# Performance work log

Measured on AMD Instinct MI355X. Metric: run time of the kernel, lower is better.

The kernel has to match this reference:

```python
import jax, jax.numpy as jnp
import numpy as np

K = 20          # neighbour_num
EMB = 512       # emb_dims
EPS = 1e-12     # guards sqrt grad at self-neighbor zero distance


def setup_inputs() -> dict:
    key = jax.random.key(0)
    ks = jax.random.split(key, 6)
    B, D, N = 8, 3, 4096
    C_in = 2 * D + K  # 26 = 6 + neighbour_num
    def xavier(k, o, c):
        return jax.random.normal(k, (o, c), jnp.float32) * jnp.sqrt(2.0 / (o + c))
    return {
        "x":  jax.random.normal(ks[0], (B, D, N), jnp.float32),
        "w1": xavier(ks[1], 64, C_in),
        "w2": xavier(ks[2], 64, 64),
        "w3": xavier(ks[3], 128, 64),
        "w4": xavier(ks[4], 256, 128),
        "w5": xavier(ks[5], EMB, 512),
    }


def _graph_feature(x):
    # x: (B, D, N). Returns (B, 2D+K, N, K).
    B, D, N = x.shape
    xt = jnp.swapaxes(x, 1, 2)                      # (B, N, D)
    sq = jnp.sum(x * x, axis=1)                     # (B, N)
    # pairwise = -||xi - xj||^2 ; topk picks nearest neighbors (incl. self)
    pair = 2.0 * jnp.einsum('bdn,bdm->bnm', x, x) - sq[:, :, None] - sq[:, None, :]
    idx = jax.lax.top_k(pair, K)[1]                 # (B, N, K) int32
    nbr = xt[jnp.arange(B)[:, None, None], idx]     # (B, N, K, D) gather
    xc = jnp.broadcast_to(xt[:, :, None, :], (B, N, K, D))
    dist = jnp.sqrt(jnp.sum((nbr - xc) ** 2, axis=-1) + EPS)   # (B, N, K)
    distr = jnp.broadcast_to(dist[:, :, None, :], (B, N, K, K))
    feat = jnp.concatenate([xc, nbr, distr], axis=-1)          # (B, N, K, 2D+K)
    return jnp.transpose(feat, (0, 3, 1, 2))        # (B, 2D+K, N, K)


def _conv1x1(h, w):
    # h: (B, C, N, K), w: (O, C)  -> (B, O, N, K)
    return jnp.einsum('bcnk,oc->bonk', h, w)


def reference(x, w1, w2, w3, w4, w5):
    h = _graph_feature(x)                           # (B, 26, N, K)
    h = jax.nn.relu(_conv1x1(h, w1)); x1 = h.max(axis=-1)   # (B, 64, N)
    h = jax.nn.relu(_conv1x1(h, w2)); x2 = h.max(axis=-1)   # (B, 64, N)
    h = jax.nn.relu(_conv1x1(h, w3)); x3 = h.max(axis=-1)   # (B, 128, N)
    h = jax.nn.relu(_conv1x1(h, w4)); x4 = h.max(axis=-1)   # (B, 256, N)
    cat = jnp.concatenate([x1, x2, x3, x4], axis=1)          # (B, 512, N)
    out = jax.nn.relu(jnp.einsum('bcn,oc->bon', cat, w5))    # (B, EMB, N)
    return out
```

## Files before the change

### kernel.cpp

```cpp
#include <hip/hip_runtime.h>
#include <cstdint>
#include <cstddef>

#define NB   8
#define NPTS 4096
#define KNN  20
#define P    4
#define QPW  4

typedef __attribute__((ext_vector_type(8))) short    short8;
typedef __attribute__((ext_vector_type(4))) float    floatx4;
typedef __attribute__((ext_vector_type(4))) unsigned short ushort4v;

__device__ __forceinline__ uint16_t f2bf(float f) {
    uint32_t u = __float_as_uint(f);
    uint32_t r = (u + 0x7FFFu + ((u >> 16) & 1u)) >> 16;
    return (uint16_t)r;
}
__device__ __forceinline__ float bf2f(uint16_t h) {
    return __uint_as_float(((uint32_t)h) << 16);
}

#define NEGINF __int_as_float((int)0xFF800000)

template <int CTRL>
__device__ __forceinline__ float dpp_maxf(float v) {
    int o = __builtin_amdgcn_update_dpp(__float_as_int(v), __float_as_int(v),
                                        CTRL, 0xF, 0xF, false);
    return fmaxf(v, __int_as_float(o));
}
__device__ __forceinline__ float wave_max_f32(float v) {
    v = dpp_maxf<0x111>(v);
    v = dpp_maxf<0x112>(v);
    v = dpp_maxf<0x114>(v);
    v = dpp_maxf<0x118>(v);
    v = dpp_maxf<0x142>(v);
    v = dpp_maxf<0x143>(v);
    return __int_as_float(__builtin_amdgcn_readlane(__float_as_int(v), 63));
}

__global__ __launch_bounds__(256) void prep_xyzs(
    const float* __restrict__ x,
    float4* __restrict__ xyzs)
{
    const int i = blockIdx.x * 256 + threadIdx.x;
    if (i >= NB * NPTS) return;
    const int b = i / NPTS, n = i - b * NPTS;
    const float* xb = x + (size_t)b * 3 * NPTS;
    const float x0 = xb[n], x1 = xb[NPTS + n], x2 = xb[2 * NPTS + n];
    float4 v;
    v.x = x0; v.y = x1; v.z = x2;
    v.w = fmaf(x2, x2, fmaf(x1, x1, x0 * x0));
    xyzs[i] = v;
}

__global__ __launch_bounds__(256) void topk_kernel(
    const float4* __restrict__ xyzs,
    int*   __restrict__ idx_out,
    float* __restrict__ dist_out)
{
    const int t = threadIdx.x;
    const int wave = t >> 6, l = t & 63;
    const int nbase = (blockIdx.x * 4 + wave) * QPW;
    const int b = blockIdx.y;
    const float4* xq = xyzs + (size_t)b * NPTS;

    float xn0[QPW], xn1[QPW], xn2[QPW], sqn[QPW];
    float V0[QPW], V1[QPW], V2[QPW];
    int   J0[QPW], J1[QPW], J2[QPW];
    unsigned long long consumed[QPW];
    int   my_m[QPW];

    #pragma unroll
    for (int p = 0; p < QPW; ++p) {
        const float4 pn = xq[nbase + p];
        xn0[p] = pn.x; xn1[p] = pn.y; xn2[p] = pn.z; sqn[p] = pn.w;
        V0[p] = NEGINF; V1[p] = NEGINF; V2[p] = NEGINF;
        J0[p] = 0; J1[p] = 0; J2[p] = 0;
        consumed[p] = 0ull;
        my_m[p] = 0;
    }

    #pragma unroll 4
    for (int j = 0; j < 64; ++j) {
        const float4 pm = xq[j * 64 + l];
        #pragma unroll
        for (int p = 0; p < QPW; ++p) {
            const float dot = fmaf(xn2[p], pm.z, fmaf(xn1[p], pm.y, xn0[p] * pm.x));
            const float s = 2.0f * dot - sqn[p] - pm.w;
            const bool c0 = s > V0[p], c1 = s > V1[p], c2 = s > V2[p];
            const float nV2 = __builtin_amdgcn_fmed3f(V1[p], V2[p], s);
            const float nV1 = __builtin_amdgcn_fmed3f(V0[p], V1[p], s);
            V0[p] = fmaxf(V0[p], s);
            V1[p] = nV1; V2[p] = nV2;
            const int tA = c1 ? J1[p] : j;
            J2[p] = c2 ? tA : J2[p];
            const int tB = c0 ? J0[p] : j;
            J1[p] = c1 ? tB : J1[p];
            J0[p] = c0 ? j : J0[p];
        }
    }

    #pragma unroll
    for (int p = 0; p < QPW; ++p) {
        for (int k = 0; k < KNN; ++k) {
            if (V0[p] == NEGINF) {
                V1[p] = NEGINF; V2[p] = NEGINF;
                for (int j = 0; j < 64; ++j) {
                    const float4 pm = xq[j * 64 + l];
                    const float dot = fmaf(xn2[p], pm.z, fmaf(xn1[p], pm.y, xn0[p] * pm.x));
                    float s = 2.0f * dot - sqn[p] - pm.w;
                    if ((consumed[p] >> j) & 1ull) s = NEGINF;
                    const bool c0 = s > V0[p], c1 = s > V1[p], c2 = s > V2[p];
                    const float nV2 = __builtin_amdgcn_fmed3f(V1[p], V2[p], s);
                    const float nV1 = __builtin_amdgcn_fmed3f(V0[p], V1[p], s);
                    V0[p] = fmaxf(V0[p], s);
                    V1[p] = nV1; V2[p] = nV2;
                    const int tA = c1 ? J1[p] : j;
                    J2[p] = c2 ? tA : J2[p];
                    const int tB = c0 ? J0[p] : j;
                    J1[p] = c1 ? tB : J1[p];
                    J0[p] = c0 ? j : J0[p];
                }
            }
            const float w = wave_max_f32(V0[p]);
            const unsigned long long own = __ballot(V0[p] == w);
            const int owner = (int)__builtin_ctzll(own);
            const int jwin  = __builtin_amdgcn_readlane(J0[p], owner);
            const int m     = jwin * 64 + owner;
            if (l == k) my_m[p] = m;
            if (l == owner) {
                consumed[p] |= 1ull << J0[p];
                V0[p] = V1[p]; V1[p] = V2[p]; V2[p] = NEGINF;
                J0[p] = J1[p]; J1[p] = J2[p];
            }
        }
    }

    #pragma unroll
    for (int p = 0; p < QPW; ++p) {
        if (l < KNN) {
            const int n = nbase + p;
            const float4 pm = xq[my_m[p]];
            const float d0 = pm.x - xn0[p], d1 = pm.y - xn1[p], d2 = pm.z - xn2[p];
            const float dist = sqrtf(((d0 * d0 + d1 * d1) + d2 * d2) + 1e-12f);
            const size_t base = ((size_t)b * NPTS + n) * KNN + l;
            idx_out[base]  = my_m[p];
            dist_out[base] = dist;
        }
    }
}

__global__ void prep_wfrag(const float* __restrict__ w, uint16_t* __restrict__ frag,
                           int C, int NT, int KT) {
    const int i = blockIdx.x * 256 + threadIdx.x;
    if (i >= NT * KT * 64) return;
    const int lane = i & 63;
    const int kt   = (i >> 6) % KT;
    const int nt   = (i >> 6) / KT;
    const int n    = nt * 16 + (lane & 15);
    const int c0   = kt * 32 + (lane >> 4) * 8;
    uint16_t o[8];
    #pragma unroll
    for (int j = 0; j < 8; ++j) {
        const int c = c0 + j;
        o[j] = (c < C) ? f2bf(w[(size_t)n * C + c]) : (uint16_t)0;
    }
    uint16_t* dst = frag + (size_t)i * 8;
    #pragma unroll
    for (int j = 0; j < 8; ++j) dst[j] = o[j];
}

__global__ __launch_bounds__(256) void prep_w5bf(const float* __restrict__ w5,
                                                 uint16_t* __restrict__ w5b) {
    const int i = blockIdx.x * 256 + threadIdx.x;
    if (i < 512 * 512) w5b[i] = f2bf(w5[i]);
}

template <int NT_TOT, int KT, int IN_STRIDE, int OUT_STRIDE>
__device__ __forceinline__ void mfma_layer(const uint16_t* __restrict__ in,
                                           uint16_t* __restrict__ out,
                                           const uint16_t* __restrict__ wf,
                                           int wave, int lane) {
    constexpr int NT_W = NT_TOT / 4;
    const int col = lane & 15, quad = lane >> 4;
    short8 bfrag[NT_W][KT];
    #pragma unroll
    for (int ni = 0; ni < NT_W; ++ni)
        #pragma unroll
        for (int k = 0; k < KT; ++k)
            bfrag[ni][k] = *(const short8*)(wf +
                ((size_t)((wave * NT_W + ni) * KT + k) * 64 + lane) * 8);
    #pragma unroll
    for (int mt = 0; mt < 5; ++mt) {
        short8 af[KT];
        #pragma unroll
        for (int k = 0; k < KT; ++k)
            af[k] = *(const short8*)(in + (mt * 16 + col) * IN_STRIDE + k * 32 + quad * 8);
        #pragma unroll
        for (int ni = 0; ni < NT_W; ++ni) {
            floatx4 acc = {0.f, 0.f, 0.f, 0.f};
            #pragma unroll
            for (int k = 0; k < KT; ++k)
                acc = __builtin_amdgcn_mfma_f32_16x16x32_bf16(af[k], bfrag[ni][k], acc, 0, 0, 0);
            const int nt = wave * NT_W + ni;
            #pragma unroll
            for (int r = 0; r < 4; ++r) {
                const float v = acc[r] > 0.f ? acc[r] : 0.f;
                out[(mt * 16 + quad * 4 + r) * OUT_STRIDE + nt * 16 + col] = f2bf(v);
            }
        }
    }
}

template <int O, int STRIDE>
__device__ __forceinline__ void maxk(const uint16_t* __restrict__ h,
                                     uint16_t* __restrict__ cat_ws, int catoff,
                                     int t, int b, int n0) {
    constexpr int G = O / 8;
    if (t < P * G) {
        const int p = t / G, g = t % G;
        uint16_t mx[8];
        #pragma unroll
        for (int j = 0; j < 8; ++j) mx[j] = 0;
        for (int k = 0; k < KNN; ++k) {
            const uint16_t* row = h + (p * KNN + k) * STRIDE + g * 8;
            #pragma unroll
            for (int j = 0; j < 8; ++j) mx[j] = row[j] > mx[j] ? row[j] : mx[j];
        }
        uint16_t* dst = cat_ws + ((size_t)b * NPTS + n0 + p) * 512 + catoff + g * 8;
        *(short8*)dst = *(const short8*)mx;
    }
}

__global__ __launch_bounds__(256) void fused_mlp_mfma(
    const float* __restrict__ x,
    const int*   __restrict__ idx_ws,
    const float* __restrict__ dist_ws,
    const uint16_t* __restrict__ wf1,
    const uint16_t* __restrict__ wf2,
    const uint16_t* __restrict__ wf3,
    const uint16_t* __restrict__ wf4,
    uint16_t* __restrict__ cat_ws)
{
    const int n0 = blockIdx.x * P, b = blockIdx.y, t = threadIdx.x;
    const int wave = t >> 6, lane = t & 63;

    __shared__ __align__(16) uint16_t bufA[12800];
    __shared__ __align__(16) uint16_t bufB[10880];

    for (int i = t; i < 1600; i += 256) ((uint32_t*)bufA)[i] = 0;
    __syncthreads();
    {
        const float* xb = x + (size_t)b * 3 * NPTS;
        if (t < P * KNN) {
            const int p = t / KNN, k = t % KNN;
            const int n = n0 + p;
            const size_t base = ((size_t)b * NPTS + n) * KNN + k;
            const int   m = idx_ws[base];
            const float d = dist_ws[base];
            uint16_t* fr = bufA + t * 40;
            fr[0] = f2bf(xb[n]);        fr[1] = f2bf(xb[NPTS + n]);
            fr[2] = f2bf(xb[2 * NPTS + n]);
            fr[3] = f2bf(xb[m]);        fr[4] = f2bf(xb[NPTS + m]);
            fr[5] = f2bf(xb[2 * NPTS + m]);
            const uint16_t db = f2bf(d);
            #pragma unroll
            for (int j = 0; j < KNN; ++j) bufA[(p * KNN + j) * 40 + 6 + k] = db;
        }
    }
    __syncthreads();

    mfma_layer<4, 1, 40, 72>(bufA, bufB, wf1, wave, lane);
    __syncthreads();

    maxk<64, 72>(bufB, cat_ws, 0, t, b, n0);
    mfma_layer<4, 2, 72, 72>(bufB, bufA, wf2, wave, lane);
    __syncthreads();

    maxk<64, 72>(bufA, cat_ws, 64, t, b, n0);
    mfma_layer<8, 2, 72, 136>(bufA, bufB, wf3, wave, lane);
    __syncthreads();

    maxk<128, 136>(bufB, cat_ws, 128, t, b, n0);
    {
        float* slab = (float*)bufA + wave * 1600;
        const int col = lane & 15, quad = lane >> 4;
        #pragma unroll
        for (int ni = 0; ni < 4; ++ni) {
            const int nt = wave * 4 + ni;
            short8 bfrag[4];
            #pragma unroll
            for (int k = 0; k < 4; ++k)
                bfrag[k] = *(const short8*)(wf4 + ((size_t)(nt * 4 + k) * 64 + lane) * 8);
            #pragma unroll
            for (int mt = 0; mt < 5; ++mt) {
                floatx4 acc = {0.f, 0.f, 0.f, 0.f};
                #pragma unroll
                for (int k = 0; k < 4; ++k) {
                    const short8 af = *(const short8*)(bufB + (mt * 16 + col) * 136
                                                           + k * 32 + quad * 8);
                    acc = __builtin_amdgcn_mfma_f32_16x16x32_bf16(af, bfrag[k], acc, 0, 0, 0);
                }
                #pragma unroll
                for (int r = 0; r < 4; ++r)
                    slab[(mt * 16 + quad * 4 + r) * 20 + col] = fmaxf(acc[r], 0.f);
            }
            const int p = lane >> 4, grp = (lane >> 2) & 3, kq = lane & 3;
            floatx4 mx = {0.f, 0.f, 0.f, 0.f};
            #pragma unroll
            for (int i = 0; i < 5; ++i) {
                const floatx4 v = *(const floatx4*)&slab[(p * KNN + kq * 5 + i) * 20 + grp * 4];
                mx[0] = fmaxf(mx[0], v[0]); mx[1] = fmaxf(mx[1], v[1]);
                mx[2] = fmaxf(mx[2], v[2]); mx[3] = fmaxf(mx[3], v[3]);
            }
            #pragma unroll
            for (int r = 0; r < 4; ++r) {
                mx[r] = fmaxf(mx[r], __shfl_xor(mx[r], 1));
                mx[r] = fmaxf(mx[r], __shfl_xor(mx[r], 2));
            }
            if (kq == 0) {
                ushort4v q;
                q.x = f2bf(mx[0]); q.y = f2bf(mx[1]);
                q.z = f2bf(mx[2]); q.w = f2bf(mx[3]);
                uint16_t* dst = cat_ws + ((size_t)b * NPTS + n0 + p) * 512
                              + 256 + nt * 16 + grp * 4;
                *(ushort4v*)dst = q;
            }
        }
    }
}

__global__ __launch_bounds__(256) void final_gemm_mfma(
    const uint16_t* __restrict__ w5b,
    const uint16_t* __restrict__ cat,
    float* __restrict__ out)
{
    const int b  = blockIdx.z;
    const int o0 = blockIdx.y * 64;
    const int n0 = blockIdx.x * 64;
    const int t  = threadIdx.x;
    const int wave = t >> 6, lane = t & 63;
    const int col = lane & 15, quad = lane >> 4;

    __shared__ __align__(16) uint16_t As[64 * 72];
    __shared__ __align__(16) uint16_t Bs[64 * 72];

    floatx4 acc[4] = {{0.f,0.f,0.f,0.f},{0.f,0.f,0.f,0.f},
                      {0.f,0.f,0.f,0.f},{0.f,0.f,0.f,0.f}};

    const size_t arow_base = (size_t)o0 * 512;
    const size_t brow_base = ((size_t)b * NPTS + n0) * 512;

    for (int kc = 0; kc < 512; kc += 64) {
        #pragma unroll
        for (int i = 0; i < 2; ++i) {
            const int idx = t + i * 256;
            const int row = idx >> 3;
            const int k8  = (idx & 7) * 8;
            *(short8*)&As[row * 72 + k8] =
                *(const short8*)&w5b[arow_base + (size_t)row * 512 + kc + k8];
            *(short8*)&Bs[row * 72 + k8] =
                *(const short8*)&cat[brow_base + (size_t)row * 512 + kc + k8];
        }
        __syncthreads();
        #pragma unroll
        for (int kt = 0; kt < 2; ++kt) {
            const short8 af = *(const short8*)&As[(wave * 16 + col) * 72 + kt * 32 + quad * 8];
            #pragma unroll
            for (int ns = 0; ns < 4; ++ns) {
                const short8 bf = *(const short8*)&Bs[(ns * 16 + col) * 72 + kt * 32 + quad * 8];
                acc[ns] = __builtin_amdgcn_mfma_f32_16x16x32_bf16(af, bf, acc[ns], 0, 0, 0);
            }
        }
        __syncthreads();
    }

    #pragma unroll
    for (int ns = 0; ns < 4; ++ns) {
        #pragma unroll
        for (int r = 0; r < 4; ++r) {
            out[((size_t)b * 512 + o0 + wave * 16 + quad * 4 + r) * NPTS
                + n0 + ns * 16 + col] = fmaxf(acc[ns][r], 0.f);
        }
    }
}

extern "C" void kernel_launch(void* const* d_in, const int* in_sizes, int n_in,
                              void* d_out, int out_size, void* d_ws, size_t ws_size,
                              hipStream_t stream) {
    const float* x  = (const float*)d_in[0];
    const float* w1 = (const float*)d_in[1];
    const float* w2 = (const float*)d_in[2];
    const float* w3 = (const float*)d_in[3];
    const float* w4 = (const float*)d_in[4];
    const float* w5 = (const float*)d_in[5];
    float* out = (float*)d_out;

    char* ws = (char*)d_ws;
    int*      idx_ws  = (int*)ws;
    float*    dist_ws = (float*)(ws + 2621440);
    uint16_t* cat_ws  = (uint16_t*)(ws + 5242880);
    float4*   xyzs    = (float4*)(ws + 5242880);
    uint16_t* w5b     = (uint16_t*)(ws + 38797312);
    uint16_t* wf1     = (uint16_t*)(ws + 72351744);
    uint16_t* wf2     = (uint16_t*)(ws + 72351744 + 4096);
    uint16_t* wf3     = (uint16_t*)(ws + 72351744 + 4096 + 8192);
    uint16_t* wf4     = (uint16_t*)(ws + 72351744 + 4096 + 8192 + 16384);

    prep_wfrag<<<dim3(1), 256, 0, stream>>>(w1, wf1, 26,  4, 1);
    prep_wfrag<<<dim3(2), 256, 0, stream>>>(w2, wf2, 64,  4, 2);
    prep_wfrag<<<dim3(4), 256, 0, stream>>>(w3, wf3, 64,  8, 2);
    prep_wfrag<<<dim3(16), 256, 0, stream>>>(w4, wf4, 128, 16, 4);
    prep_w5bf<<<dim3(1024), 256, 0, stream>>>(w5, w5b);
    prep_xyzs<<<dim3((NB * NPTS + 255) / 256), 256, 0, stream>>>(x, xyzs);

    topk_kernel<<<dim3(NPTS / (4 * QPW), NB), 256, 0, stream>>>(xyzs, idx_ws, dist_ws);
    fused_mlp_mfma<<<dim3(NPTS / P, NB), 256, 0, stream>>>(
        x, idx_ws, dist_ws, wf1, wf2, wf3, wf4, cat_ws);
    final_gemm_mfma<<<dim3(NPTS / 64, 512 / 64, NB), 256, 0, stream>>>(w5b, cat_ws, out);
}
```

Baseline: 372.5 us.

## Stage batch points in LDS for top-k and interleave per-query selection rounds

The top-k kernel now uses 1024-thread blocks that load all 4096 points of a batch into shared memory once, then scan from LDS instead of global memory. Query coordinates are made wave-uniform with readfirstlane. The per-lane consumed bitmask is dropped and rebuilt from already-selected indices only when a lane's refill runs, which cuts register pressure. The k and query loops are swapped so the four wave-max reductions can overlap. Costs are 64KB of LDS per block, which limits blocks per CU, and a refill path that now loops over prior picks.

```diff
diff --git a/kernel.cpp b/kernel.cpp
--- a/kernel.cpp
+++ b/kernel.cpp
@@ -7,6 +7,7 @@
 #define KNN  20
 #define P    4
 #define QPW  4
+#define WPB  16
 
 typedef __attribute__((ext_vector_type(8))) short    short8;
 typedef __attribute__((ext_vector_type(4))) float    floatx4;
@@ -22,6 +23,10 @@
 }
 
 #define NEGINF __int_as_float((int)0xFF800000)
+
+__device__ __forceinline__ float rfl_f32(float v) {
+    return __uint_as_float((uint32_t)__builtin_amdgcn_readfirstlane(__float_as_uint(v)));
+}
 
 template <int CTRL>
 __device__ __forceinline__ float dpp_maxf(float v) {
@@ -54,36 +59,40 @@
     xyzs[i] = v;
 }
 
-__global__ __launch_bounds__(256) void topk_kernel(
+__global__ __launch_bounds__(1024, 8) void topk_kernel(
     const float4* __restrict__ xyzs,
     int*   __restrict__ idx_out,
     float* __restrict__ dist_out)
 {
     const int t = threadIdx.x;
     const int wave = t >> 6, l = t & 63;
-    const int nbase = (blockIdx.x * 4 + wave) * QPW;
     const int b = blockIdx.y;
     const float4* xq = xyzs + (size_t)b * NPTS;
+
+    __shared__ float4 pts[NPTS];
+    for (int i = t; i < NPTS; i += WPB * 64) pts[i] = xq[i];
+    __syncthreads();
+
+    const int nbase = (blockIdx.x * WPB + wave) * QPW;
 
     float xn0[QPW], xn1[QPW], xn2[QPW], sqn[QPW];
     float V0[QPW], V1[QPW], V2[QPW];
     int   J0[QPW], J1[QPW], J2[QPW];
-    unsigned long long consumed[QPW];
     int   my_m[QPW];
 
     #pragma unroll
     for (int p = 0; p < QPW; ++p) {
-        const float4 pn = xq[nbase + p];
-        xn0[p] = pn.x; xn1[p] = pn.y; xn2[p] = pn.z; sqn[p] = pn.w;
+        const float4 pn = pts[nbase + p];
+        xn0[p] = rfl_f32(pn.x); xn1[p] = rfl_f32(pn.y);
+        xn2[p] = rfl_f32(pn.z); sqn[p] = rfl_f32(pn.w);
         V0[p] = NEGINF; V1[p] = NEGINF; V2[p] = NEGINF;
         J0[p] = 0; J1[p] = 0; J2[p] = 0;
-        consumed[p] = 0ull;
         my_m[p] = 0;
     }
 
-    #pragma unroll 4
+    #pragma unroll 2
     for (int j = 0; j < 64; ++j) {
-        const float4 pm = xq[j * 64 + l];
+        const float4 pm = pts[j * 64 + l];
         #pragma unroll
         for (int p = 0; p < QPW; ++p) {
             const float dot = fmaf(xn2[p], pm.z, fmaf(xn1[p], pm.y, xn0[p] * pm.x));
@@ -101,16 +110,21 @@
         }
     }
 
-    #pragma unroll
-    for (int p = 0; p < QPW; ++p) {
-        for (int k = 0; k < KNN; ++k) {
+    for (int k = 0; k < KNN; ++k) {
+        #pragma unroll
+        for (int p = 0; p < QPW; ++p) {
             if (V0[p] == NEGINF) {
+                unsigned long long cons = 0ull;
+                for (int i = 0; i < k; ++i) {
+                    const int mw = __builtin_amdgcn_readlane(my_m[p], i);
+                    if ((mw & 63) == l) cons |= 1ull << (mw >> 6);
+                }
                 V1[p] = NEGINF; V2[p] = NEGINF;
                 for (int j = 0; j < 64; ++j) {
-                    const float4 pm = xq[j * 64 + l];
+                    const float4 pm = pts[j * 64 + l];
                     const float dot = fmaf(xn2[p], pm.z, fmaf(xn1[p], pm.y, xn0[p] * pm.x));
                     float s = 2.0f * dot - sqn[p] - pm.w;
-                    if ((consumed[p] >> j) & 1ull) s = NEGINF;
+                    if ((cons >> j) & 1ull) s = NEGINF;
                     const bool c0 = s > V0[p], c1 = s > V1[p], c2 = s > V2[p];
                     const float nV2 = __builtin_amdgcn_fmed3f(V1[p], V2[p], s);
                     const float nV1 = __builtin_amdgcn_fmed3f(V0[p], V1[p], s);
@@ -123,14 +137,18 @@
                     J0[p] = c0 ? j : J0[p];
                 }
             }
-            const float w = wave_max_f32(V0[p]);
-            const unsigned long long own = __ballot(V0[p] == w);
+        }
+        float wv[QPW];
+        #pragma unroll
+        for (int p = 0; p < QPW; ++p) wv[p] = wave_max_f32(V0[p]);
+        #pragma unroll
+        for (int p = 0; p < QPW; ++p) {
+            const unsigned long long own = __ballot(V0[p] == wv[p]);
             const int owner = (int)__builtin_ctzll(own);
             const int jwin  = __builtin_amdgcn_readlane(J0[p], owner);
             const int m     = jwin * 64 + owner;
             if (l == k) my_m[p] = m;
             if (l == owner) {
-                consumed[p] |= 1ull << J0[p];
                 V0[p] = V1[p]; V1[p] = V2[p]; V2[p] = NEGINF;
                 J0[p] = J1[p]; J1[p] = J2[p];
             }
@@ -141,7 +159,7 @@
     for (int p = 0; p < QPW; ++p) {
         if (l < KNN) {
             const int n = nbase + p;
-            const float4 pm = xq[my_m[p]];
+            const float4 pm = pts[my_m[p]];
             const float d0 = pm.x - xn0[p], d1 = pm.y - xn1[p], d2 = pm.z - xn2[p];
             const float dist = sqrtf(((d0 * d0 + d1 * d1) + d2 * d2) + 1e-12f);
             const size_t base = ((size_t)b * NPTS + n) * KNN + l;
@@ -415,7 +433,7 @@
     prep_w5bf<<<dim3(1024), 256, 0, stream>>>(w5, w5b);
     prep_xyzs<<<dim3((NB * NPTS + 255) / 256), 256, 0, stream>>>(x, xyzs);
 
-    topk_kernel<<<dim3(NPTS / (4 * QPW), NB), 256, 0, stream>>>(xyzs, idx_ws, dist_ws);
+    topk_kernel<<<dim3(NPTS / (WPB * QPW), NB), 1024, 0, stream>>>(xyzs, idx_ws, dist_ws);
     fused_mlp_mfma<<<dim3(NPTS / P, NB), 256, 0, stream>>>(
         x, idx_ws, dist_ws, wf1, wf2, wf3, wf4, cat_ws);
     final_gemm_mfma<<<dim3(NPTS / 64, 512 / 64, NB), 256, 0, stream>>>(w5b, cat_ws, out);
```

After: 374.9 us. Within noise of the previous version (+0.7%).
